# Performance work log

Measured on AMD Instinct MI355X. Metric: run time of the kernel, lower is better.

The kernel has to match this reference:

```python
import jax, jax.numpy as jnp
import numpy as np

B, S, D = 2048, 8, 1280
K = 1                 # n_components_remove
HIGH_T = 0.6          # PC1_HIGH_ACTIVITY_THRESHOLD
STORM_T = 0.8         # solar_storm_threshold


def setup_inputs() -> dict:
    key = jax.random.key(0)
    k1, k2 = jax.random.split(key, 2)
    features = jax.random.normal(k1, (B, S, D), dtype=jnp.float32)
    kp_index = jax.random.uniform(k2, (B,), dtype=jnp.float32) * 9.0
    cmr_gate = jnp.ones((1,), dtype=jnp.float32)  # nn.Parameter(torch.ones(1))
    return {"features": features, "kp_index": kp_index, "cmr_gate": cmr_gate}


def reference(features, kp_index, cmr_gate):
    # Per-sample standardization over the feature axis (numpy std, ddof=0)
    mu = features.mean(axis=2, keepdims=True)            # (B, S, 1)
    sigma = features.std(axis=2, keepdims=True) + 1e-8   # (B, S, 1)
    fn = (features - mu) / sigma                         # (B, S, D)

    # Batched thin SVD of the (S, D) normalized feature matrix
    U, sv, Vt = jnp.linalg.svd(fn, full_matrices=False)  # (B,S,S), (B,S), (B,S,D)
    var = sv * sv
    pc1_ratio = var[:, 0] / (var.sum(axis=-1) + 1e-8)    # (B,)

    # solar_flag: 0 normal, 1 high activity, 2 storm
    solar_flag = (pc1_ratio >= HIGH_T).astype(jnp.int32) + (pc1_ratio >= STORM_T).astype(jnp.int32)

    # Rank-K reconstruction of the common-mode (solar) component
    low = jnp.einsum('bsk,bk,bkd->bsd', U[:, :, :K], sv[:, :K], Vt[:, :K, :])
    clean = (fn - low) * sigma + mu                      # de-normalized cleaned features

    # Kp-gating: amplify CMR when Kp >= 5
    kp_gate = 1.0 + 0.5 * (kp_index >= 5.0).astype(features.dtype)[:, None, None]
    clean = features + kp_gate * (clean - features)

    # Learnable gate
    gate = jax.nn.sigmoid(cmr_gate)[0]
    features_clean = features + gate * (clean - features)
    return features_clean, pc1_ratio, solar_flag
```

## Files before the change

### kernel.cpp

```cpp
#include <hip/hip_runtime.h>
#include <math.h>


#define SV 8
#define DV 1280
#define BSTRIDE (SV*DV)
#define HALF 640
#define NCH 5

__device__ __forceinline__ float wsum(float v) {
    v += __shfl_xor(v, 32);
    v += __shfl_xor(v, 16);
    v += __shfl_xor(v, 8);
    v += __shfl_xor(v, 4);
    v += __shfl_xor(v, 2);
    v += __shfl_xor(v, 1);
    return v;
}

#define GU(i,k) ((i) <= (k) ? G[i][k] : G[k][i])
#define AU(i,k) ((i) <= (k) ? A[i][k] : A[k][i])

__global__ __launch_bounds__(128, 2)
void cmr_dual(const float* __restrict__ feat,
              const float* __restrict__ kp,
              const float* __restrict__ cmr_gate,
              float* __restrict__ out, int Bn)
{
    __shared__ float xch[52];
    __shared__ float cf[17];

    const int tid  = threadIdx.x;
    const int lane = tid & 63;
    const int w    = tid >> 6;
    const int b    = blockIdx.x;

    const float* __restrict__ fb =
        feat + (size_t)b * BSTRIDE + w * HALF + lane * 2;

    float G[8][8];
    float S[8];
#pragma unroll
    for (int i = 0; i < 8; ++i) {
        S[i] = 0.f;
#pragma unroll
        for (int j = i; j < 8; ++j) G[i][j] = 0.f;
    }
#pragma unroll
    for (int c = 0; c < NCH; ++c) {
        float2 x[8];
#pragma unroll
        for (int s = 0; s < 8; ++s)
            x[s] = *(const float2*)(fb + (size_t)s * DV + c * 128);
#pragma unroll
        for (int i = 0; i < 8; ++i) {
            S[i] += x[i].x + x[i].y;
#pragma unroll
            for (int j = i; j < 8; ++j)
                G[i][j] = fmaf(x[i].x, x[j].x,
                          fmaf(x[i].y, x[j].y, G[i][j]));
        }
    }
#pragma unroll
    for (int i = 0; i < 8; ++i) {
        S[i] = wsum(S[i]);
#pragma unroll
        for (int j = i; j < 8; ++j) G[i][j] = wsum(G[i][j]);
    }

    if (w == 1 && lane == 0) {
        int p = 0;
#pragma unroll
        for (int i = 0; i < 8; ++i)
#pragma unroll
            for (int j = i; j < 8; ++j) { xch[p] = G[i][j]; ++p; }
#pragma unroll
        for (int i = 0; i < 8; ++i) xch[44 + i] = S[i];
    }
    __syncthreads();

    if (w == 0) {
        {
            int p = 0;
#pragma unroll
            for (int i = 0; i < 8; ++i)
#pragma unroll
                for (int j = i; j < 8; ++j) { G[i][j] += xch[p]; ++p; }
#pragma unroll
            for (int i = 0; i < 8; ++i) S[i] += xch[44 + i];
        }

        float mu[8], sig[8], rsig[8];
        const float invD = 1.f / (float)DV;
#pragma unroll
        for (int i = 0; i < 8; ++i) {
            mu[i] = S[i] * invD;
            const float var = fmaxf(G[i][i] * invD - mu[i] * mu[i], 0.f);
            sig[i]  = sqrtf(var) + 1e-8f;
            rsig[i] = 1.f / sig[i];
        }
#pragma unroll
        for (int i = 0; i < 8; ++i)
#pragma unroll
            for (int j = i; j < 8; ++j)
                G[i][j] = (G[i][j] - (float)DV * mu[i] * mu[j]) * rsig[i] * rsig[j];

        float tr = 0.f;
#pragma unroll
        for (int i = 0; i < 8; ++i) tr += G[i][i];

        float A[8][8];
        {
            const float rt = 1.f / fmaxf(tr, 1e-30f);
#pragma unroll
            for (int i = 0; i < 8; ++i)
#pragma unroll
                for (int j = i; j < 8; ++j) A[i][j] = G[i][j] * rt;
        }
#pragma unroll
        for (int t = 0; t < 12; ++t) {
            float Bm[8][8];
            float trB = 0.f;
#pragma unroll
            for (int i = 0; i < 8; ++i)
#pragma unroll
                for (int j = i; j < 8; ++j) {
                    float acc = 0.f;
#pragma unroll
                    for (int k = 0; k < 8; ++k)
                        acc = fmaf(AU(i, k), AU(j, k), acc);
                    Bm[i][j] = acc;
                    if (i == j) trB += acc;
                }
            const float rt = 1.f / fmaxf(trB, 1e-30f);
#pragma unroll
            for (int i = 0; i < 8; ++i)
#pragma unroll
                for (int j = i; j < 8; ++j) A[i][j] = Bm[i][j] * rt;
        }
        int bj = 0; float best = A[0][0];
#pragma unroll
        for (int k = 1; k < 8; ++k)
            if (A[k][k] > best) { best = A[k][k]; bj = k; }
        float u[8];
#pragma unroll
        for (int i = 0; i < 8; ++i) {
            float v = AU(i, 0);
#pragma unroll
            for (int k = 1; k < 8; ++k) v = (bj == k) ? AU(i, k) : v;
            u[i] = v;
        }
        {
            float nn = 0.f;
#pragma unroll
            for (int i = 0; i < 8; ++i) nn = fmaf(u[i], u[i], nn);
            const float r = rsqrtf(fmaxf(nn, 1e-30f));
#pragma unroll
            for (int i = 0; i < 8; ++i) u[i] *= r;
        }
#pragma unroll
        for (int it = 0; it < 2; ++it) {
            float y[8]; float ny = 0.f;
#pragma unroll
            for (int i = 0; i < 8; ++i) {
                float acc = 0.f;
#pragma unroll
                for (int k = 0; k < 8; ++k) acc = fmaf(GU(i, k), u[k], acc);
                y[i] = acc; ny = fmaf(acc, acc, ny);
            }
            const float r = rsqrtf(fmaxf(ny, 1e-30f));
#pragma unroll
            for (int i = 0; i < 8; ++i) u[i] = y[i] * r;
        }
        float lam = 0.f;
#pragma unroll
        for (int i = 0; i < 8; ++i) {
            float acc = 0.f;
#pragma unroll
            for (int k = 0; k < 8; ++k) acc = fmaf(GU(i, k), u[k], acc);
            lam = fmaf(u[i], acc, lam);
        }
        const float pc1 = lam / (tr + 1e-8f);

        const float gate = 1.f / (1.f + expf(-cmr_gate[0]));
        const float kpg  = (kp[b] >= 5.0f) ? 1.5f : 1.0f;
        const float Gt   = gate * kpg;

        float eav[8], ecv[8];
#pragma unroll
        for (int i = 0; i < 8; ++i) {
            eav[i] = u[i] * rsig[i];
            ecv[i] = Gt * sig[i] * u[i];
        }
        float ebc = 0.f;
#pragma unroll
        for (int i = 0; i < 8; ++i) ebc = fmaf(eav[i], mu[i], ebc);

        if (lane == 0) {
#pragma unroll
            for (int i = 0; i < 8; ++i) { cf[i] = eav[i]; cf[8 + i] = ecv[i]; }
            cf[16] = ebc;
            out[(size_t)Bn * BSTRIDE + b] = pc1;
            out[(size_t)Bn * BSTRIDE + Bn + b] =
                (pc1 >= 0.6f ? 1.f : 0.f) + (pc1 >= 0.8f ? 1.f : 0.f);
        }
    }
    __syncthreads();

    float av[8], cv[8];
#pragma unroll
    for (int s = 0; s < 8; ++s) { av[s] = cf[s]; cv[s] = cf[8 + s]; }
    const float bc = cf[16];

    float* __restrict__ ob = out + (size_t)b * BSTRIDE + w * HALF + lane * 2;

#pragma unroll
    for (int c = 0; c < NCH; ++c) {
        float2 x[8];
#pragma unroll
        for (int s = 0; s < 8; ++s)
            x[s] = *(const float2*)(fb + (size_t)s * DV + c * 128);

        float2 p = make_float2(-bc, -bc);
#pragma unroll
        for (int s = 0; s < 8; ++s) {
            p.x = fmaf(av[s], x[s].x, p.x);
            p.y = fmaf(av[s], x[s].y, p.y);
        }
#pragma unroll
        for (int s = 0; s < 8; ++s) {
            float2 o;
            o.x = fmaf(-cv[s], p.x, x[s].x);
            o.y = fmaf(-cv[s], p.y, x[s].y);
            *(float2*)(ob + (size_t)s * DV + c * 128) = o;
        }
    }
}

extern "C" void kernel_launch(void* const* d_in, const int* in_sizes, int n_in,
                              void* d_out, int out_size, void* d_ws, size_t ws_size,
                              hipStream_t stream) {
    const float* feat = (const float*)d_in[0];
    const float* kp   = (const float*)d_in[1];
    const float* gate = (const float*)d_in[2];
    float* out = (float*)d_out;
    const int Bn = in_sizes[0] / BSTRIDE;
    (void)d_ws; (void)ws_size;

    cmr_dual<<<Bn, 128, 0, stream>>>(feat, kp, gate, out, Bn);
}
```

Baseline: 175.2 us.

## Split fused kernel into gram, batched eigen, and apply kernels

```diff
diff --git a/kernel.cpp b/kernel.cpp
--- a/kernel.cpp
+++ b/kernel.cpp
@@ -4,9 +4,8 @@
 
 #define SV 8
 #define DV 1280
+#define D4 320
 #define BSTRIDE (SV*DV)
-#define HALF 640
-#define NCH 5
 
 __device__ __forceinline__ float wsum(float v) {
     v += __shfl_xor(v, 32);
@@ -21,22 +20,13 @@
 #define GU(i,k) ((i) <= (k) ? G[i][k] : G[k][i])
 #define AU(i,k) ((i) <= (k) ? A[i][k] : A[k][i])
 
-__global__ __launch_bounds__(128, 2)
-void cmr_dual(const float* __restrict__ feat,
-              const float* __restrict__ kp,
-              const float* __restrict__ cmr_gate,
-              float* __restrict__ out, int Bn)
+__global__ __launch_bounds__(64)
+void cmr_gram(const float* __restrict__ feat, float* __restrict__ gws, int Bn)
 {
-    __shared__ float xch[52];
-    __shared__ float cf[17];
-
-    const int tid  = threadIdx.x;
-    const int lane = tid & 63;
-    const int w    = tid >> 6;
+    const int lane = threadIdx.x;
     const int b    = blockIdx.x;
 
-    const float* __restrict__ fb =
-        feat + (size_t)b * BSTRIDE + w * HALF + lane * 2;
+    const float* __restrict__ fb = feat + (size_t)b * BSTRIDE + lane * 2;
 
     float G[8][8];
     float S[8];
@@ -47,7 +37,7 @@
         for (int j = i; j < 8; ++j) G[i][j] = 0.f;
     }
 #pragma unroll
-    for (int c = 0; c < NCH; ++c) {
+    for (int c = 0; c < 10; ++c) {
         float2 x[8];
 #pragma unroll
         for (int s = 0; s < 8; ++s)
@@ -67,173 +57,188 @@
 #pragma unroll
         for (int j = i; j < 8; ++j) G[i][j] = wsum(G[i][j]);
     }
-
-    if (w == 1 && lane == 0) {
+    if (lane == 0) {
         int p = 0;
 #pragma unroll
         for (int i = 0; i < 8; ++i)
 #pragma unroll
-            for (int j = i; j < 8; ++j) { xch[p] = G[i][j]; ++p; }
-#pragma unroll
-        for (int i = 0; i < 8; ++i) xch[44 + i] = S[i];
-    }
-    __syncthreads();
-
-    if (w == 0) {
-        {
-            int p = 0;
-#pragma unroll
-            for (int i = 0; i < 8; ++i)
-#pragma unroll
-                for (int j = i; j < 8; ++j) { G[i][j] += xch[p]; ++p; }
-#pragma unroll
-            for (int i = 0; i < 8; ++i) S[i] += xch[44 + i];
-        }
-
-        float mu[8], sig[8], rsig[8];
-        const float invD = 1.f / (float)DV;
-#pragma unroll
-        for (int i = 0; i < 8; ++i) {
-            mu[i] = S[i] * invD;
-            const float var = fmaxf(G[i][i] * invD - mu[i] * mu[i], 0.f);
-            sig[i]  = sqrtf(var) + 1e-8f;
-            rsig[i] = 1.f / sig[i];
-        }
-#pragma unroll
-        for (int i = 0; i < 8; ++i)
-#pragma unroll
-            for (int j = i; j < 8; ++j)
-                G[i][j] = (G[i][j] - (float)DV * mu[i] * mu[j]) * rsig[i] * rsig[j];
-
-        float tr = 0.f;
-#pragma unroll
-        for (int i = 0; i < 8; ++i) tr += G[i][i];
-
-        float A[8][8];
-        {
-            const float rt = 1.f / fmaxf(tr, 1e-30f);
-#pragma unroll
-            for (int i = 0; i < 8; ++i)
-#pragma unroll
-                for (int j = i; j < 8; ++j) A[i][j] = G[i][j] * rt;
-        }
-#pragma unroll
-        for (int t = 0; t < 12; ++t) {
-            float Bm[8][8];
-            float trB = 0.f;
-#pragma unroll
-            for (int i = 0; i < 8; ++i)
-#pragma unroll
-                for (int j = i; j < 8; ++j) {
-                    float acc = 0.f;
-#pragma unroll
-                    for (int k = 0; k < 8; ++k)
-                        acc = fmaf(AU(i, k), AU(j, k), acc);
-                    Bm[i][j] = acc;
-                    if (i == j) trB += acc;
-                }
-            const float rt = 1.f / fmaxf(trB, 1e-30f);
-#pragma unroll
-            for (int i = 0; i < 8; ++i)
-#pragma unroll
-                for (int j = i; j < 8; ++j) A[i][j] = Bm[i][j] * rt;
-        }
-        int bj = 0; float best = A[0][0];
-#pragma unroll
-        for (int k = 1; k < 8; ++k)
-            if (A[k][k] > best) { best = A[k][k]; bj = k; }
-        float u[8];
-#pragma unroll
-        for (int i = 0; i < 8; ++i) {
-            float v = AU(i, 0);
-#pragma unroll
-            for (int k = 1; k < 8; ++k) v = (bj == k) ? AU(i, k) : v;
-            u[i] = v;
-        }
-        {
-            float nn = 0.f;
-#pragma unroll
-            for (int i = 0; i < 8; ++i) nn = fmaf(u[i], u[i], nn);
-            const float r = rsqrtf(fmaxf(nn, 1e-30f));
-#pragma unroll
-            for (int i = 0; i < 8; ++i) u[i] *= r;
-        }
-#pragma unroll
-        for (int it = 0; it < 2; ++it) {
-            float y[8]; float ny = 0.f;
-#pragma unroll
-            for (int i = 0; i < 8; ++i) {
+            for (int j = i; j < 8; ++j) { gws[(size_t)p * Bn + b] = G[i][j]; ++p; }
+#pragma unroll
+        for (int i = 0; i < 8; ++i) gws[(size_t)(44 + i) * Bn + b] = S[i];
+    }
+}
+
+__global__ __launch_bounds__(64, 1)
+void cmr_eigen(const float* __restrict__ gws,
+               const float* __restrict__ kp,
+               const float* __restrict__ cmr_gate,
+               float* __restrict__ cf,
+               float* __restrict__ out, int Bn)
+{
+    const int b = blockIdx.x * 64 + threadIdx.x;
+
+    float G[8][8], S[8], mu[8], sig[8], rsig[8];
+    {
+        int p = 0;
+#pragma unroll
+        for (int i = 0; i < 8; ++i)
+#pragma unroll
+            for (int j = i; j < 8; ++j) { G[i][j] = gws[(size_t)p * Bn + b]; ++p; }
+#pragma unroll
+        for (int i = 0; i < 8; ++i) S[i] = gws[(size_t)(44 + i) * Bn + b];
+    }
+    const float invD = 1.f / (float)DV;
+#pragma unroll
+    for (int i = 0; i < 8; ++i) {
+        mu[i] = S[i] * invD;
+        const float var = fmaxf(G[i][i] * invD - mu[i] * mu[i], 0.f);
+        sig[i]  = sqrtf(var) + 1e-8f;
+        rsig[i] = 1.f / sig[i];
+    }
+#pragma unroll
+    for (int i = 0; i < 8; ++i)
+#pragma unroll
+        for (int j = i; j < 8; ++j)
+            G[i][j] = (G[i][j] - (float)DV * mu[i] * mu[j]) * rsig[i] * rsig[j];
+
+    float tr = 0.f;
+#pragma unroll
+    for (int i = 0; i < 8; ++i) tr += G[i][i];
+
+    float A[8][8];
+    {
+        const float rt = 1.f / fmaxf(tr, 1e-30f);
+#pragma unroll
+        for (int i = 0; i < 8; ++i)
+#pragma unroll
+            for (int j = i; j < 8; ++j) A[i][j] = G[i][j] * rt;
+    }
+#pragma unroll
+    for (int t = 0; t < 12; ++t) {
+        float Bm[8][8];
+        float trB = 0.f;
+#pragma unroll
+        for (int i = 0; i < 8; ++i)
+#pragma unroll
+            for (int j = i; j < 8; ++j) {
                 float acc = 0.f;
 #pragma unroll
-                for (int k = 0; k < 8; ++k) acc = fmaf(GU(i, k), u[k], acc);
-                y[i] = acc; ny = fmaf(acc, acc, ny);
+                for (int k = 0; k < 8; ++k)
+                    acc = fmaf(AU(i, k), AU(j, k), acc);
+                Bm[i][j] = acc;
+                if (i == j) trB += acc;
             }
-            const float r = rsqrtf(fmaxf(ny, 1e-30f));
-#pragma unroll
-            for (int i = 0; i < 8; ++i) u[i] = y[i] * r;
-        }
-        float lam = 0.f;
+        const float rt = 1.f / fmaxf(trB, 1e-30f);
+#pragma unroll
+        for (int i = 0; i < 8; ++i)
+#pragma unroll
+            for (int j = i; j < 8; ++j) A[i][j] = Bm[i][j] * rt;
+    }
+    int bj = 0; float best = A[0][0];
+#pragma unroll
+    for (int k = 1; k < 8; ++k)
+        if (A[k][k] > best) { best = A[k][k]; bj = k; }
+    float u[8];
+#pragma unroll
+    for (int i = 0; i < 8; ++i) {
+        float v = AU(i, 0);
+#pragma unroll
+        for (int k = 1; k < 8; ++k) v = (bj == k) ? AU(i, k) : v;
+        u[i] = v;
+    }
+    {
+        float nn = 0.f;
+#pragma unroll
+        for (int i = 0; i < 8; ++i) nn = fmaf(u[i], u[i], nn);
+        const float r = rsqrtf(fmaxf(nn, 1e-30f));
+#pragma unroll
+        for (int i = 0; i < 8; ++i) u[i] *= r;
+    }
+#pragma unroll
+    for (int it = 0; it < 2; ++it) {
+        float y[8]; float ny = 0.f;
 #pragma unroll
         for (int i = 0; i < 8; ++i) {
             float acc = 0.f;
 #pragma unroll
             for (int k = 0; k < 8; ++k) acc = fmaf(GU(i, k), u[k], acc);
-            lam = fmaf(u[i], acc, lam);
+            y[i] = acc; ny = fmaf(acc, acc, ny);
         }
-        const float pc1 = lam / (tr + 1e-8f);
-
-        const float gate = 1.f / (1.f + expf(-cmr_gate[0]));
-        const float kpg  = (kp[b] >= 5.0f) ? 1.5f : 1.0f;
-        const float Gt   = gate * kpg;
-
-        float eav[8], ecv[8];
-#pragma unroll
-        for (int i = 0; i < 8; ++i) {
-            eav[i] = u[i] * rsig[i];
-            ecv[i] = Gt * sig[i] * u[i];
-        }
-        float ebc = 0.f;
-#pragma unroll
-        for (int i = 0; i < 8; ++i) ebc = fmaf(eav[i], mu[i], ebc);
-
-        if (lane == 0) {
-#pragma unroll
-            for (int i = 0; i < 8; ++i) { cf[i] = eav[i]; cf[8 + i] = ecv[i]; }
-            cf[16] = ebc;
-            out[(size_t)Bn * BSTRIDE + b] = pc1;
-            out[(size_t)Bn * BSTRIDE + Bn + b] =
-                (pc1 >= 0.6f ? 1.f : 0.f) + (pc1 >= 0.8f ? 1.f : 0.f);
-        }
-    }
-    __syncthreads();
-
-    float av[8], cv[8];
-#pragma unroll
-    for (int s = 0; s < 8; ++s) { av[s] = cf[s]; cv[s] = cf[8 + s]; }
-    const float bc = cf[16];
-
-    float* __restrict__ ob = out + (size_t)b * BSTRIDE + w * HALF + lane * 2;
-
-#pragma unroll
-    for (int c = 0; c < NCH; ++c) {
-        float2 x[8];
-#pragma unroll
-        for (int s = 0; s < 8; ++s)
-            x[s] = *(const float2*)(fb + (size_t)s * DV + c * 128);
-
-        float2 p = make_float2(-bc, -bc);
-#pragma unroll
-        for (int s = 0; s < 8; ++s) {
-            p.x = fmaf(av[s], x[s].x, p.x);
-            p.y = fmaf(av[s], x[s].y, p.y);
-        }
-#pragma unroll
-        for (int s = 0; s < 8; ++s) {
-            float2 o;
-            o.x = fmaf(-cv[s], p.x, x[s].x);
-            o.y = fmaf(-cv[s], p.y, x[s].y);
-            *(float2*)(ob + (size_t)s * DV + c * 128) = o;
-        }
+        const float r = rsqrtf(fmaxf(ny, 1e-30f));
+#pragma unroll
+        for (int i = 0; i < 8; ++i) u[i] = y[i] * r;
+    }
+    float lam = 0.f;
+#pragma unroll
+    for (int i = 0; i < 8; ++i) {
+        float acc = 0.f;
+#pragma unroll
+        for (int k = 0; k < 8; ++k) acc = fmaf(GU(i, k), u[k], acc);
+        lam = fmaf(u[i], acc, lam);
+    }
+    const float pc1 = lam / (tr + 1e-8f);
+
+    const float gate = 1.f / (1.f + expf(-cmr_gate[0]));
+    const float kpg  = (kp[b] >= 5.0f) ? 1.5f : 1.0f;
+    const float Gt   = gate * kpg;
+
+    float bc = 0.f;
+#pragma unroll
+    for (int i = 0; i < 8; ++i) bc = fmaf(u[i] * rsig[i], mu[i], bc);
+
+#pragma unroll
+    for (int i = 0; i < 8; ++i) {
+        cf[(size_t)i * Bn + b]       = u[i] * rsig[i];
+        cf[(size_t)(8 + i) * Bn + b] = Gt * sig[i] * u[i];
+    }
+    cf[(size_t)16 * Bn + b] = bc;
+    out[(size_t)Bn * BSTRIDE + b] = pc1;
+    out[(size_t)Bn * BSTRIDE + Bn + b] =
+        (pc1 >= 0.6f ? 1.f : 0.f) + (pc1 >= 0.8f ? 1.f : 0.f);
+}
+
+__global__ __launch_bounds__(320)
+void cmr_apply(const float* __restrict__ feat,
+               const float* __restrict__ cf,
+               float* __restrict__ out, int Bn)
+{
+    const int tid  = threadIdx.x;
+    const int lane = tid & 63;
+    const int wq   = tid >> 6;
+    const int b    = blockIdx.x;
+
+    float a[8], c[8];
+#pragma unroll
+    for (int s = 0; s < 8; ++s) {
+        a[s] = cf[(size_t)s * Bn + b];
+        c[s] = cf[(size_t)(8 + s) * Bn + b];
+    }
+    const float bc = cf[(size_t)16 * Bn + b];
+
+    const float4* __restrict__ f4 = (const float4*)(feat + (size_t)b * BSTRIDE);
+    float4* __restrict__ o4 = (float4*)(out + (size_t)b * BSTRIDE);
+    const int d4 = wq * 64 + lane;
+
+    float4 f[8];
+#pragma unroll
+    for (int s = 0; s < 8; ++s) f[s] = f4[s * D4 + d4];
+
+    float4 p = make_float4(-bc, -bc, -bc, -bc);
+#pragma unroll
+    for (int s = 0; s < 8; ++s) {
+        p.x = fmaf(a[s], f[s].x, p.x);
+        p.y = fmaf(a[s], f[s].y, p.y);
+        p.z = fmaf(a[s], f[s].z, p.z);
+        p.w = fmaf(a[s], f[s].w, p.w);
+    }
+#pragma unroll
+    for (int s = 0; s < 8; ++s) {
+        float4 o;
+        o.x = fmaf(-c[s], p.x, f[s].x);
+        o.y = fmaf(-c[s], p.y, f[s].y);
+        o.z = fmaf(-c[s], p.z, f[s].z);
+        o.w = fmaf(-c[s], p.w, f[s].w);
+        o4[s * D4 + d4] = o;
     }
 }
 
@@ -245,7 +250,11 @@
     const float* gate = (const float*)d_in[2];
     float* out = (float*)d_out;
     const int Bn = in_sizes[0] / BSTRIDE;
-    (void)d_ws; (void)ws_size;
-
-    cmr_dual<<<Bn, 128, 0, stream>>>(feat, kp, gate, out, Bn);
-}
+
+    float* gws = (float*)d_ws;
+    float* cf  = gws + (size_t)52 * Bn;
+
+    cmr_gram <<<Bn,      64,  0, stream>>>(feat, gws, Bn);
+    cmr_eigen<<<Bn / 64, 64,  0, stream>>>(gws, kp, gate, cf, out, Bn);
+    cmr_apply<<<Bn,      320, 0, stream>>>(feat, cf, out, Bn);
+}
```

Result: no change. 176.7 us (+0.8%).
